# Kernel optimization log

Hardware: AMD Instinct MI355X
Metric: run time of the kernel (lower is better)

## Reference

```python
import jax, jax.numpy as jnp
import numpy as np
import math

S, B, H, NH = 2048, 2, 2048, 16
HN = H // NH  # head dim = 128

def setup_inputs() -> dict:
    key = jax.random.key(0)
    ks = jax.random.split(key, 5)
    hidden_states = jax.random.normal(ks[0], (S, B, H), dtype=jnp.float32)
    # causal mask: True means masked (filled with -10000), broadcast over heads
    attention_mask = jnp.triu(jnp.ones((S, S), dtype=bool), k=1)[None, None].repeat(B, axis=0)
    w_qkv = jax.random.normal(ks[1], (3 * H, H), dtype=jnp.float32) * (1.0 / math.sqrt(H))
    b_qkv = jax.random.normal(ks[2], (3 * H,), dtype=jnp.float32) * 0.02
    w_dense = jax.random.normal(ks[3], (H, H), dtype=jnp.float32) * (1.0 / math.sqrt(H))
    b_dense = jax.random.normal(ks[4], (H,), dtype=jnp.float32) * 0.02
    return {"hidden_states": hidden_states, "attention_mask": attention_mask,
            "w_qkv": w_qkv, "b_qkv": b_qkv, "w_dense": w_dense, "b_dense": b_dense}

def reference(hidden_states, attention_mask, w_qkv, b_qkv, w_dense, b_dense):
    s, b, h = hidden_states.shape
    nh, hn = NH, h // NH
    # QKV projection (ColumnParallelLinear, world_size=1)
    qkv = hidden_states @ w_qkv.T + b_qkv                # [s, b, 3h]
    qkv = qkv.reshape(s, b, nh, 3 * hn)
    q, k, v = jnp.split(qkv, 3, axis=-1)                 # each [s, b, nh, hn]
    q = q.transpose(1, 2, 0, 3)                          # [b, nh, s, hn]
    k = k.transpose(1, 2, 0, 3)
    v = v.transpose(1, 2, 0, 3)
    # norm_factor = sqrt(hn)*coeff, softmax rescales by coeff -> net 1/sqrt(hn)
    scores = jnp.einsum('bnqh,bnkh->bnqk', q, k) / jnp.float32(math.sqrt(hn))
    scores = jnp.where(attention_mask, jnp.float32(-10000.0), scores)
    probs = jax.nn.softmax(scores, axis=-1)              # [b, nh, s, s]
    ctx = jnp.einsum('bnqk,bnkh->bnqh', probs, v)        # [b, nh, s, hn]
    ctx = ctx.transpose(2, 0, 1, 3).reshape(s, b, h)     # [s, b, h]
    # RowParallelLinear with skip_bias_add=True: bias returned separately
    output = ctx @ w_dense.T
    return output, b_dense
```

## Files before the change

### kernel.cpp

```cpp
#include <hip/hip_runtime.h>

typedef unsigned short u16;
typedef unsigned int   u32;
typedef __attribute__((ext_vector_type(8))) short bf16x8;
typedef __attribute__((ext_vector_type(4))) float f32x4;

#define S_LEN 2048
#define B_SZ  2
#define H_DIM 2048
#define NH_   16
#define HN_   128
#define M_TOK 4096
#define NQKV  6144
#define NT_   (S_LEN / 64)

__device__ __forceinline__ u16 f2bf(float f) {
    u32 x = __float_as_uint(f);
    return (u16)((x + 0x7fffu + ((x >> 16) & 1u)) >> 16);
}

__device__ __forceinline__ void async16(const void* g, void* l) {
    __builtin_amdgcn_global_load_lds((const __attribute__((address_space(1))) void*)g,
                                     (__attribute__((address_space(3))) void*)l,
                                     16, 0, 0);
}

__global__ __launch_bounds__(256) void cvt_bf16(const float* __restrict__ in,
                                                u16* __restrict__ out, int n) {
    int i = (blockIdx.x * 256 + threadIdx.x) * 4;
    if (i + 3 < n) {
        float4 v = *(const float4*)&in[i];
        ushort4 o;
        o.x = f2bf(v.x); o.y = f2bf(v.y); o.z = f2bf(v.z); o.w = f2bf(v.w);
        *(ushort4*)&out[i] = o;
    }
}

template<int EPI>
__global__ __launch_bounds__(256) void gemm_mfma(
    const u16* __restrict__ A, const u16* __restrict__ W,
    const float* __restrict__ bias, float* __restrict__ Cout,
    u16* __restrict__ Qb, u16* __restrict__ Kb, u16* __restrict__ Vt,
    int M, int N, int K)
{
    __shared__ __align__(16) u16 Af[16 * 64 * 8];
    __shared__ __align__(16) u16 Bf[16 * 64 * 8];
    const int t = threadIdx.x, l = t & 63, w = t >> 6;
    const int quad = l >> 4, ln = l & 15;
    const int wm = w >> 1, wn = w & 1;
    const int m0 = blockIdx.y * 128, n0 = blockIdx.x * 128;

    f32x4 acc[4][4];
#pragma unroll
    for (int i = 0; i < 4; ++i)
#pragma unroll
        for (int j = 0; j < 4; ++j)
#pragma unroll
            for (int r = 0; r < 4; ++r) acc[i][j][r] = 0.f;

    for (int k0 = 0; k0 < K; k0 += 64) {
#pragma unroll
        for (int i = 0; i < 4; ++i) {
            int c  = i * 4 + w;
            int mb = c >> 1, ks = c & 1;
            async16(&A[(size_t)(m0 + mb * 16 + ln) * K + k0 + ks * 32 + quad * 8],
                    &Af[(c * 64 + l) * 8]);
            async16(&W[(size_t)(n0 + mb * 16 + ln) * K + k0 + ks * 32 + quad * 8],
                    &Bf[(c * 64 + l) * 8]);
        }
        __syncthreads();
        bf16x8 af[4][2], bfr[4][2];
#pragma unroll
        for (int x = 0; x < 4; ++x)
#pragma unroll
            for (int ks = 0; ks < 2; ++ks) {
                af[x][ks]  = *(const bf16x8*)&Af[((((wm * 4 + x) * 2) + ks) * 64 + l) * 8];
                bfr[x][ks] = *(const bf16x8*)&Bf[((((wn * 4 + x) * 2) + ks) * 64 + l) * 8];
            }
#pragma unroll
        for (int mt = 0; mt < 4; ++mt)
#pragma unroll
            for (int nt = 0; nt < 4; ++nt)
#pragma unroll
                for (int ks = 0; ks < 2; ++ks)
                    acc[mt][nt] = __builtin_amdgcn_mfma_f32_16x16x32_bf16(
                        af[mt][ks], bfr[nt][ks], acc[mt][nt], 0, 0, 0);
        __syncthreads();
    }

    if constexpr (EPI == 0) {
#pragma unroll
        for (int mt = 0; mt < 4; ++mt)
#pragma unroll
            for (int nt = 0; nt < 4; ++nt) {
                int col = n0 + (wn * 4 + nt) * 16 + ln;
#pragma unroll
                for (int r = 0; r < 4; ++r) {
                    int row = m0 + wm * 64 + mt * 16 + quad * 4 + r;
                    Cout[(size_t)row * N + col] = acc[mt][nt][r];
                }
            }
    } else {
        const float kQS = 0.08838834764831845f * 1.44269504088896340f;
#pragma unroll
        for (int nt = 0; nt < 4; ++nt) {
            int col  = n0 + (wn * 4 + nt) * 16 + ln;
            int head = col / 384;
            int g    = col - head * 384;
            int sec  = g >> 7;
            int d    = g & 127;
            float bv = bias[col];
#pragma unroll
            for (int mt = 0; mt < 4; ++mt)
#pragma unroll
                for (int r = 0; r < 4; ++r) {
                    int tok = m0 + wm * 64 + mt * 16 + quad * 4 + r;
                    int s = tok >> 1, bb = tok & 1;
                    float v = acc[mt][nt][r] + bv;
                    if (sec == 0)
                        Qb[((size_t)(bb * NH_ + head) * S_LEN + s) * HN_ + d] = f2bf(v * kQS);
                    else if (sec == 1)
                        Kb[((size_t)(bb * NH_ + head) * S_LEN + s) * HN_ + d] = f2bf(v);
                    else
                        Vt[((size_t)(bb * NH_ + head) * HN_ + d) * S_LEN + s] = f2bf(v);
                }
        }
    }
}

__global__ __launch_bounds__(256) void attn_mfma(
    const u16* __restrict__ Qb, const u16* __restrict__ Kb,
    const u16* __restrict__ Vt, u16* __restrict__ Ctx)
{
    __shared__ __align__(16) u16 Ks[2][16 * 64 * 8];
    __shared__ __align__(16) u16 Vs[2][16 * 64 * 8];
    __shared__ __align__(16) u16 Psm[4][16][72];

    const int t = threadIdx.x, l = t & 63, w = t >> 6;
    const int quad = l >> 4, ln = l & 15;
    const int j = blockIdx.x;
    const int n = blockIdx.y, b = blockIdx.z;
    const u16* Qh = Qb + (size_t)(b * NH_ + n) * S_LEN * HN_;
    const u16* Kh = Kb + (size_t)(b * NH_ + n) * S_LEN * HN_;
    const u16* Vh = Vt + (size_t)(b * NH_ + n) * HN_ * S_LEN;

#pragma unroll 1
    for (int phase = 0; phase < 2; ++phase) {
        const int qt = phase ? j : (NT_ - 1 - j);
        const int q0 = qt * 64;

#pragma unroll
        for (int i = 0; i < 4; ++i)
            async16(&Qh[(size_t)(q0 + i * 16 + ln) * HN_ + w * 32 + quad * 8],
                    &Ks[1][((i * 4 + w) * 64 + l) * 8]);
#pragma unroll
        for (int i = 0; i < 4; ++i) {
            async16(&Kh[(size_t)(i * 16 + ln) * HN_ + w * 32 + quad * 8],
                    &Ks[0][((i * 4 + w) * 64 + l) * 8]);
            int dv = i * 4 + w, dt = dv >> 1, ks = dv & 1;
            async16(&Vh[(size_t)(dt * 16 + ln) * S_LEN + ks * 32 + quad * 8],
                    &Vs[0][(dv * 64 + l) * 8]);
        }
        __syncthreads();

        bf16x8 qf[4];
#pragma unroll
        for (int ks = 0; ks < 4; ++ks)
            qf[ks] = *(const bf16x8*)&Ks[1][((w * 4 + ks) * 64 + l) * 8];
        __syncthreads();

        float m_i[4], l_i[4];
        f32x4 acco[8];
#pragma unroll
        for (int r = 0; r < 4; ++r) { m_i[r] = -1e30f; l_i[r] = 0.f; }
#pragma unroll
        for (int dt = 0; dt < 8; ++dt)
#pragma unroll
            for (int r = 0; r < 4; ++r) acco[dt][r] = 0.f;

#pragma unroll 1
        for (int kt = 0; kt <= qt; ++kt) {
            const int cur = kt & 1;

            if (kt < qt) {
                const int nxt = cur ^ 1;
#pragma unroll
                for (int i = 0; i < 4; ++i) {
                    async16(&Kh[(size_t)((kt + 1) * 64 + i * 16 + ln) * HN_ + w * 32 + quad * 8],
                            &Ks[nxt][((i * 4 + w) * 64 + l) * 8]);
                    int dv = i * 4 + w, dt = dv >> 1, ks = dv & 1;
                    async16(&Vh[(size_t)(dt * 16 + ln) * S_LEN + (kt + 1) * 64 + ks * 32 + quad * 8],
                            &Vs[nxt][(dv * 64 + l) * 8]);
                }
            }

            f32x4 sc[4];
#pragma unroll
            for (int nt = 0; nt < 4; ++nt)
#pragma unroll
                for (int r = 0; r < 4; ++r) sc[nt][r] = 0.f;
#pragma unroll
            for (int nt = 0; nt < 4; ++nt)
#pragma unroll
                for (int ks = 0; ks < 4; ++ks) {
                    bf16x8 kf = *(const bf16x8*)&Ks[cur][((nt * 4 + ks) * 64 + l) * 8];
                    sc[nt] = __builtin_amdgcn_mfma_f32_16x16x32_bf16(qf[ks], kf, sc[nt], 0, 0, 0);
                }

            if (kt == qt) {
#pragma unroll
                for (int nt = 0; nt < 4; ++nt)
#pragma unroll
                    for (int r = 0; r < 4; ++r)
                        if (nt * 16 + ln > w * 16 + quad * 4 + r) sc[nt][r] = -1e30f;
            }

            float corr[4];
#pragma unroll
            for (int r = 0; r < 4; ++r) {
                float mx = fmaxf(fmaxf(sc[0][r], sc[1][r]), fmaxf(sc[2][r], sc[3][r]));
                mx = fmaxf(mx, __shfl_xor(mx, 1));
                mx = fmaxf(mx, __shfl_xor(mx, 2));
                mx = fmaxf(mx, __shfl_xor(mx, 4));
                mx = fmaxf(mx, __shfl_xor(mx, 8));
                float mnew = fmaxf(m_i[r], mx);
                corr[r] = exp2f(m_i[r] - mnew);
                m_i[r] = mnew;
            }
#pragma unroll
            for (int r = 0; r < 4; ++r) {
                float ps = 0.f;
#pragma unroll
                for (int nt = 0; nt < 4; ++nt) {
                    float p = exp2f(sc[nt][r] - m_i[r]);
                    ps += p;
                    Psm[w][quad * 4 + r][nt * 16 + ln] = f2bf(p);
                }
                l_i[r] = l_i[r] * corr[r] + ps;
            }

#pragma unroll
            for (int dt = 0; dt < 8; ++dt)
#pragma unroll
                for (int r = 0; r < 4; ++r) acco[dt][r] *= corr[r];

            bf16x8 pf[2];
#pragma unroll
            for (int ks = 0; ks < 2; ++ks)
                pf[ks] = *(const bf16x8*)&Psm[w][ln][ks * 32 + quad * 8];
#pragma unroll
            for (int dt = 0; dt < 8; ++dt)
#pragma unroll
                for (int ks = 0; ks < 2; ++ks) {
                    bf16x8 vf = *(const bf16x8*)&Vs[cur][((dt * 2 + ks) * 64 + l) * 8];
                    acco[dt] = __builtin_amdgcn_mfma_f32_16x16x32_bf16(pf[ks], vf, acco[dt], 0, 0, 0);
                }
            __syncthreads();
        }

#pragma unroll
        for (int r = 0; r < 4; ++r) {
            float s = l_i[r];
            s += __shfl_xor(s, 1);
            s += __shfl_xor(s, 2);
            s += __shfl_xor(s, 4);
            s += __shfl_xor(s, 8);
            l_i[r] = 1.f / s;
        }
#pragma unroll
        for (int dt = 0; dt < 8; ++dt)
#pragma unroll
            for (int r = 0; r < 4; ++r) {
                int srow = q0 + w * 16 + quad * 4 + r;
                Ctx[((size_t)(srow * B_SZ + b)) * H_DIM + n * HN_ + dt * 16 + ln] =
                    f2bf(acco[dt][r] * l_i[r]);
            }
    }
}

__global__ void copy_bias(const float* __restrict__ b_dense, float* __restrict__ out)
{
    int t = blockIdx.x * 256 + threadIdx.x;
    if (t < H_DIM) out[(size_t)M_TOK * H_DIM + t] = b_dense[t];
}

extern "C" void kernel_launch(void* const* d_in, const int* in_sizes, int n_in,
                              void* d_out, int out_size, void* d_ws, size_t ws_size,
                              hipStream_t stream)
{
    const float* hs      = (const float*)d_in[0];
    const float* w_qkv   = (const float*)d_in[2];
    const float* b_qkv   = (const float*)d_in[3];
    const float* w_dense = (const float*)d_in[4];
    const float* b_dense = (const float*)d_in[5];
    float* out = (float*)d_out;

    u16* hs_bf = (u16*)d_ws;
    u16* wq_bf = hs_bf + (size_t)M_TOK * H_DIM;
    u16* wd_bf = wq_bf + (size_t)NQKV * H_DIM;
    u16* Qb    = wd_bf + (size_t)H_DIM * H_DIM;
    u16* Kb    = Qb    + (size_t)M_TOK * H_DIM;
    u16* Vt    = Kb    + (size_t)M_TOK * H_DIM;
    u16* Ctx   = Vt    + (size_t)M_TOK * H_DIM;

    cvt_bf16<<<(M_TOK * H_DIM) / 1024, 256, 0, stream>>>(hs, hs_bf, M_TOK * H_DIM);
    cvt_bf16<<<(NQKV * H_DIM) / 1024, 256, 0, stream>>>(w_qkv, wq_bf, NQKV * H_DIM);
    cvt_bf16<<<(H_DIM * H_DIM) / 1024, 256, 0, stream>>>(w_dense, wd_bf, H_DIM * H_DIM);

    gemm_mfma<1><<<dim3(NQKV / 128, M_TOK / 128), 256, 0, stream>>>(
        hs_bf, wq_bf, b_qkv, nullptr, Qb, Kb, Vt, M_TOK, NQKV, H_DIM);

    attn_mfma<<<dim3(NT_ / 2, NH_, B_SZ), 256, 0, stream>>>(Qb, Kb, Vt, Ctx);

    gemm_mfma<0><<<dim3(H_DIM / 128, M_TOK / 128), 256, 0, stream>>>(
        Ctx, wd_bf, nullptr, out, nullptr, nullptr, nullptr, M_TOK, H_DIM, H_DIM);

    copy_bias<<<(H_DIM + 255) / 256, 256, 0, stream>>>(b_dense, out);
}
```

Measured before the change: 518.9 us.

## Double-buffer GEMM LDS tiles with BK=32 and merge bf16 conversion launches

```diff
diff --git a/kernel.cpp b/kernel.cpp
--- a/kernel.cpp
+++ b/kernel.cpp
@@ -25,15 +25,22 @@
                                      16, 0, 0);
 }
 
-__global__ __launch_bounds__(256) void cvt_bf16(const float* __restrict__ in,
-                                                u16* __restrict__ out, int n) {
-    int i = (blockIdx.x * 256 + threadIdx.x) * 4;
-    if (i + 3 < n) {
-        float4 v = *(const float4*)&in[i];
-        ushort4 o;
-        o.x = f2bf(v.x); o.y = f2bf(v.y); o.z = f2bf(v.z); o.w = f2bf(v.w);
-        *(ushort4*)&out[i] = o;
-    }
+__global__ __launch_bounds__(256) void cvt3(
+    const float* __restrict__ a, u16* __restrict__ oa, int na,
+    const float* __restrict__ b, u16* __restrict__ ob, int nb,
+    const float* __restrict__ c, u16* __restrict__ oc, int nc)
+{
+    int g = blockIdx.x * 256 + threadIdx.x;
+    const float* in; u16* out; int idx;
+    if (g < na)           { in = a; out = oa; idx = g; }
+    else if (g < na + nb) { in = b; out = ob; idx = g - na; }
+    else if (g < na + nb + nc) { in = c; out = oc; idx = g - na - nb; }
+    else return;
+    int i = idx * 4;
+    float4 v = *(const float4*)&in[i];
+    ushort4 o;
+    o.x = f2bf(v.x); o.y = f2bf(v.y); o.z = f2bf(v.z); o.w = f2bf(v.w);
+    *(ushort4*)&out[i] = o;
 }
 
 template<int EPI>
@@ -43,8 +50,8 @@
     u16* __restrict__ Qb, u16* __restrict__ Kb, u16* __restrict__ Vt,
     int M, int N, int K)
 {
-    __shared__ __align__(16) u16 Af[16 * 64 * 8];
-    __shared__ __align__(16) u16 Bf[16 * 64 * 8];
+    __shared__ __align__(16) u16 Af[2][8 * 64 * 8];
+    __shared__ __align__(16) u16 Bf[2][8 * 64 * 8];
     const int t = threadIdx.x, l = t & 63, w = t >> 6;
     const int quad = l >> 4, ln = l & 15;
     const int wm = w >> 1, wn = w & 1;
@@ -58,33 +65,38 @@
 #pragma unroll
             for (int r = 0; r < 4; ++r) acc[i][j][r] = 0.f;
 
-    for (int k0 = 0; k0 < K; k0 += 64) {
-#pragma unroll
-        for (int i = 0; i < 4; ++i) {
-            int c  = i * 4 + w;
-            int mb = c >> 1, ks = c & 1;
-            async16(&A[(size_t)(m0 + mb * 16 + ln) * K + k0 + ks * 32 + quad * 8],
-                    &Af[(c * 64 + l) * 8]);
-            async16(&W[(size_t)(n0 + mb * 16 + ln) * K + k0 + ks * 32 + quad * 8],
-                    &Bf[(c * 64 + l) * 8]);
-        }
-        __syncthreads();
-        bf16x8 af[4][2], bfr[4][2];
-#pragma unroll
-        for (int x = 0; x < 4; ++x)
-#pragma unroll
-            for (int ks = 0; ks < 2; ++ks) {
-                af[x][ks]  = *(const bf16x8*)&Af[((((wm * 4 + x) * 2) + ks) * 64 + l) * 8];
-                bfr[x][ks] = *(const bf16x8*)&Bf[((((wn * 4 + x) * 2) + ks) * 64 + l) * 8];
-            }
+    auto stage = [&](int buf, int k0) {
+#pragma unroll
+        for (int i = 0; i < 2; ++i) {
+            int mb = i * 4 + w;
+            async16(&A[(size_t)(m0 + mb * 16 + ln) * K + k0 + quad * 8],
+                    &Af[buf][(mb * 64 + l) * 8]);
+            async16(&W[(size_t)(n0 + mb * 16 + ln) * K + k0 + quad * 8],
+                    &Bf[buf][(mb * 64 + l) * 8]);
+        }
+    };
+
+    stage(0, 0);
+    __syncthreads();
+
+    const int NIT = K / 32;
+#pragma unroll 1
+    for (int kk = 0; kk < NIT; ++kk) {
+        const int cur = kk & 1;
+        if (kk + 1 < NIT) stage(cur ^ 1, (kk + 1) * 32);
+
+        bf16x8 af[4], bfr[4];
+#pragma unroll
+        for (int x = 0; x < 4; ++x) {
+            af[x]  = *(const bf16x8*)&Af[cur][((wm * 4 + x) * 64 + l) * 8];
+            bfr[x] = *(const bf16x8*)&Bf[cur][((wn * 4 + x) * 64 + l) * 8];
+        }
 #pragma unroll
         for (int mt = 0; mt < 4; ++mt)
 #pragma unroll
             for (int nt = 0; nt < 4; ++nt)
-#pragma unroll
-                for (int ks = 0; ks < 2; ++ks)
-                    acc[mt][nt] = __builtin_amdgcn_mfma_f32_16x16x32_bf16(
-                        af[mt][ks], bfr[nt][ks], acc[mt][nt], 0, 0, 0);
+                acc[mt][nt] = __builtin_amdgcn_mfma_f32_16x16x32_bf16(
+                    af[mt], bfr[nt], acc[mt][nt], 0, 0, 0);
         __syncthreads();
     }
 
@@ -303,9 +315,11 @@
     u16* Vt    = Kb    + (size_t)M_TOK * H_DIM;
     u16* Ctx   = Vt    + (size_t)M_TOK * H_DIM;
 
-    cvt_bf16<<<(M_TOK * H_DIM) / 1024, 256, 0, stream>>>(hs, hs_bf, M_TOK * H_DIM);
-    cvt_bf16<<<(NQKV * H_DIM) / 1024, 256, 0, stream>>>(w_qkv, wq_bf, NQKV * H_DIM);
-    cvt_bf16<<<(H_DIM * H_DIM) / 1024, 256, 0, stream>>>(w_dense, wd_bf, H_DIM * H_DIM);
+    const int g1 = (M_TOK * H_DIM) / 4;
+    const int g2 = (NQKV * H_DIM) / 4;
+    const int g3 = (H_DIM * H_DIM) / 4;
+    cvt3<<<(g1 + g2 + g3 + 255) / 256, 256, 0, stream>>>(
+        hs, hs_bf, g1, w_qkv, wq_bf, g2, w_dense, wd_bf, g3);
 
     gemm_mfma<1><<<dim3(NQKV / 128, M_TOK / 128), 256, 0, stream>>>(
         hs_bf, wq_bf, b_qkv, nullptr, Qb, Kb, Vt, M_TOK, NQKV, H_DIM);
```

Result: faster. 507.3 us (-2.2%).
